# Kernel optimization log

Measured on AMD Instinct MI355X. Metric: run time of the kernel, lower is better.

## Reference

```python
import jax, jax.numpy as jnp
import numpy as np

MIN_PTS = 4

def setup_inputs() -> dict:
    key = jax.random.key(0)
    ks = jax.random.split(key, 10)
    P, N = 2048, 256            # proposals, max points per proposal slot
    H1, H2, OUT = 64, 128, 256  # PointNet MLP widths, extractor out_dim
    points = jax.random.normal(ks[0], (P, N, 3), dtype=jnp.float32)
    lengths = jax.random.randint(ks[1], (P,), 0, N, dtype=jnp.int32)  # some < MIN_PTS -> invalid
    centers = jax.random.normal(ks[2], (P, 3), dtype=jnp.float32) * 10.0
    sizes = jax.random.uniform(ks[3], (P, 3), minval=0.5, maxval=4.0, dtype=jnp.float32)
    proposals = jnp.concatenate([centers, sizes], axis=1)  # (P, 6)
    def lin(k, fan_in, fan_out):
        return jax.random.normal(k, (fan_in, fan_out), dtype=jnp.float32) * np.float32(1.0 / np.sqrt(fan_in))
    return {
        'points': points, 'lengths': lengths, 'proposals': proposals,
        'W1': lin(ks[4], 3, H1),   'b1': jnp.zeros((H1,), jnp.float32),
        'W2': lin(ks[5], H1, H2),  'b2': jnp.zeros((H2,), jnp.float32),
        'W3': lin(ks[6], H2, OUT), 'b3': jnp.zeros((OUT,), jnp.float32),
        'Wc': lin(ks[7], OUT, 1),  'bc': jnp.zeros((1,), jnp.float32),
        'Wr': lin(ks[8], OUT, 4),  'br': jnp.zeros((4,), jnp.float32),
    }

def reference(points, lengths, proposals, W1, b1, W2, b2, W3, b3, Wc, bc, Wr, br):
    P, N, _ = points.shape
    # repeat-padding: point i of proposal p maps to index i % n_p (gather form of the torch loop)
    L = jnp.maximum(lengths, 1)
    idx = jnp.arange(N, dtype=lengths.dtype)[None, :] % L[:, None]          # (P, N)
    batched = jnp.take_along_axis(points, idx[:, :, None], axis=1)         # (P, N, 3)
    # MultiPositionExtractor: box-normalized coords -> pointwise MLP -> max-pool
    centers = proposals[:, :3]
    half = proposals[:, 3:] * 0.5 + 1e-6
    local = (batched - centers[:, None, :]) / half[:, None, :]             # (P, N, 3)
    h = jax.nn.relu(local @ W1 + b1)                                       # (P, N, 64)
    h = jax.nn.relu(h @ W2 + b2)                                           # (P, N, 128)
    h = jax.nn.relu(h @ W3 + b3)                                           # (P, N, 256)
    feats = jnp.max(h, axis=1)                                             # (P, 256)
    # scatter-back: proposals with < MIN_PTS points get zero feature vector
    valid = lengths >= MIN_PTS
    feats = jnp.where(valid[:, None], feats, jnp.zeros((), feats.dtype))
    cls_logits = feats @ Wc + bc                                           # (P, 1)
    reg_deltas = feats @ Wr + br                                           # (P, 4)
    return cls_logits, reg_deltas
```

## Files before the change

kernel.cpp:

```cpp
#include <hip/hip_runtime.h>
#include <hip/hip_bf16.h>

#define MIN_PTS 4

typedef short bf16x8 __attribute__((ext_vector_type(8)));
typedef float f32x4  __attribute__((ext_vector_type(4)));

__device__ __forceinline__ ushort f2bf(float x) {
    unsigned u = __float_as_uint(x);
    u = (u + 0x7fffu + ((u >> 16) & 1u)) >> 16;
    return (ushort)u;
}

__device__ __forceinline__ uint cvt_pk_bf16(float lo, float hi) {
    union { __hip_bfloat162 h; uint u; } cv;
    cv.h = __float22bfloat162_rn(make_float2(lo, hi));
    return cv.u;
}

__global__ void pack_weights(const float* __restrict__ W2, const float* __restrict__ W3,
                             ushort* __restrict__ B2P, ushort* __restrict__ B3P)
{
    int idx = blockIdx.x * 256 + threadIdx.x;
    if (idx < 8192) {
        int j = idx & 7, l = (idx >> 3) & 63, ks = (idx >> 9) & 1, nt = idx >> 10;
        int k   = ks * 32 + (l >> 4) * 8 + j;
        int col = nt * 16 + (l & 15);
        B2P[idx] = f2bf(W2[k * 128 + col]);
    }
    if (idx < 32768) {
        int j = idx & 7, l = (idx >> 3) & 63, ks = (idx >> 9) & 3, nt = idx >> 11;
        int k   = ks * 32 + (l >> 4) * 8 + j;
        int col = nt * 16 + (l & 15);
        B3P[idx] = f2bf(W3[k * 256 + col]);
    }
}

__global__ __launch_bounds__(512, 4) void refine_loop(
    const float* __restrict__ points,
    const int*   __restrict__ lengths,
    const float* __restrict__ proposals,
    const float* __restrict__ W1, const float* __restrict__ b1,
    const float* __restrict__ b2,
    const float* __restrict__ b3,
    const ushort* __restrict__ B2P, const ushort* __restrict__ B3P,
    int* __restrict__ featsG,
    int P, int N, int work, int NB)
{
    __shared__ __align__(16) ushort A1[4096];
    __shared__ __align__(16) ushort A3[8192];

    const int tid  = threadIdx.x;
    const int lane = tid & 63;
    const int wu   = __builtin_amdgcn_readfirstlane(tid >> 6);
    const int rc   = lane & 15;
    const int g    = lane >> 4;

    float w1a[8], w1b[8], w1c[8], b1r[8];
    #pragma unroll
    for (int i = 0; i < 8; ++i) {
        const int f = wu * 8 + i;
        w1a[i] = W1[f]; w1b[i] = W1[64 + f]; w1c[i] = W1[128 + f]; b1r[i] = b1[f];
    }
    f32x4 bias2q;
    #pragma unroll
    for (int rr = 0; rr < 4; ++rr) bias2q[rr] = b2[16 * wu + 4 * g + rr];
    const float b3v0 = b3[16 * (2 * wu + 0) + rc];
    const float b3v1 = b3[16 * (2 * wu + 1) + rc];

    ushort* const a1wr = &A1[(((lane >> 4) * 2 + (wu >> 2)) * 64 + (wu & 3) * 16 + rc) * 8];
    const int ks3 = wu >> 1;
    const int g3  = (2 * wu + (g >> 1)) & 3;

    int q = blockIdx.x;
    int   lenC;
    float prC[6];
    float p0C, p1C, p2C;
    {
        const int pp = q >> 2, ss = q & 3;
        lenC = lengths[pp];
        #pragma unroll
        for (int i = 0; i < 6; ++i) prC[i] = proposals[pp * 6 + i];
        const int jj = min(ss * 64 + lane, max(lenC, 1) - 1);
        const float* pt = points + ((long)pp * N + jj) * 3;
        p0C = pt[0]; p1C = pt[1]; p2C = pt[2];
    }

    while (q < work) {
        const int   pcur   = q >> 2;
        const bool  active = (lenC >= MIN_PTS) && ((q & 3) * 64 < lenC);
        float pr[6];
        #pragma unroll
        for (int i = 0; i < 6; ++i) pr[i] = prC[i];
        const float p0 = p0C, p1 = p1C, p2 = p2C;

        const int qn = q + NB;
        if (qn < work) {
            const int pp = qn >> 2, ss = qn & 3;
            lenC = lengths[pp];
            #pragma unroll
            for (int i = 0; i < 6; ++i) prC[i] = proposals[pp * 6 + i];
            const int jj = min(ss * 64 + lane, max(lenC, 1) - 1);
            const float* pt = points + ((long)pp * N + jj) * 3;
            p0C = pt[0]; p1C = pt[1]; p2C = pt[2];
        }

        if (active) {
            {
                const float rx = __builtin_amdgcn_rcpf(fmaf(pr[3], 0.5f, 1e-6f));
                const float ry = __builtin_amdgcn_rcpf(fmaf(pr[4], 0.5f, 1e-6f));
                const float rz = __builtin_amdgcn_rcpf(fmaf(pr[5], 0.5f, 1e-6f));
                const float x0 = (p0 - pr[0]) * rx;
                const float x1 = (p1 - pr[1]) * ry;
                const float x2 = (p2 - pr[2]) * rz;
                float v[8];
                #pragma unroll
                for (int i = 0; i < 8; ++i)
                    v[i] = fmaxf(fmaf(x0, w1a[i], fmaf(x1, w1b[i], fmaf(x2, w1c[i], b1r[i]))), 0.f);
                uint4 qq;
                qq.x = cvt_pk_bf16(v[0], v[1]);
                qq.y = cvt_pk_bf16(v[2], v[3]);
                qq.z = cvt_pk_bf16(v[4], v[5]);
                qq.w = cvt_pk_bf16(v[6], v[7]);
                *(uint4*)a1wr = qq;
            }
            __syncthreads();

            {
                f32x4 acc2[4];
                #pragma unroll
                for (int mt = 0; mt < 4; ++mt) acc2[mt] = bias2q;

                #pragma unroll
                for (int ks = 0; ks < 2; ++ks) {
                    const bf16x8 bw = *(const bf16x8*)(B2P + ((wu * 2 + ks) * 64 + lane) * 8);
                    #pragma unroll
                    for (int mt = 0; mt < 4; ++mt) {
                        const bf16x8 a = *(const bf16x8*)&A1[((mt * 2 + ks) * 64 + lane) * 8];
                        acc2[mt] = __builtin_amdgcn_mfma_f32_16x16x32_bf16(bw, a, acc2[mt], 0, 0, 0);
                    }
                }
                #pragma unroll
                for (int mt = 0; mt < 4; ++mt) {
                    const uint u0 = cvt_pk_bf16(fmaxf(acc2[mt][0], 0.f), fmaxf(acc2[mt][1], 0.f));
                    const uint u1 = cvt_pk_bf16(fmaxf(acc2[mt][2], 0.f), fmaxf(acc2[mt][3], 0.f));
                    const int chunk = (mt * 4 + ks3) * 64 + g3 * 16 + rc;
                    uint2 val; val.x = u0; val.y = u1;
                    *(uint2*)&A3[chunk * 8 + (g & 1) * 4] = val;
                }
            }
            __syncthreads();

            {
                f32x4 acc3a[4], acc3b[4];
                #pragma unroll
                for (int mt = 0; mt < 4; ++mt) {
                    acc3a[mt] = (f32x4){b3v0, b3v0, b3v0, b3v0};
                    acc3b[mt] = (f32x4){b3v1, b3v1, b3v1, b3v1};
                }
                #pragma unroll
                for (int ks = 0; ks < 4; ++ks) {
                    const bf16x8 bf0 = *(const bf16x8*)(B3P + (((2 * wu + 0) * 4 + ks) * 64 + lane) * 8);
                    const bf16x8 bf1 = *(const bf16x8*)(B3P + (((2 * wu + 1) * 4 + ks) * 64 + lane) * 8);
                    #pragma unroll
                    for (int mt = 0; mt < 4; ++mt) {
                        const bf16x8 a = *(const bf16x8*)&A3[((mt * 4 + ks) * 64 + lane) * 8];
                        acc3a[mt] = __builtin_amdgcn_mfma_f32_16x16x32_bf16(a, bf0, acc3a[mt], 0, 0, 0);
                        acc3b[mt] = __builtin_amdgcn_mfma_f32_16x16x32_bf16(a, bf1, acc3b[mt], 0, 0, 0);
                    }
                }
                float pool0 = 0.f, pool1 = 0.f;
                #pragma unroll
                for (int mt = 0; mt < 4; ++mt)
                    #pragma unroll
                    for (int rr = 0; rr < 4; ++rr) {
                        pool0 = fmaxf(pool0, acc3a[mt][rr]);
                        pool1 = fmaxf(pool1, acc3b[mt][rr]);
                    }
                pool0 = fmaxf(pool0, __shfl_xor(pool0, 16, 64));
                pool0 = fmaxf(pool0, __shfl_xor(pool0, 32, 64));
                pool1 = fmaxf(pool1, __shfl_xor(pool1, 16, 64));
                pool1 = fmaxf(pool1, __shfl_xor(pool1, 32, 64));
                if (g == 0) {
                    atomicMax(&featsG[pcur * 256 + (2 * wu + 0) * 16 + rc], __float_as_int(pool0));
                    atomicMax(&featsG[pcur * 256 + (2 * wu + 1) * 16 + rc], __float_as_int(pool1));
                }
            }
        }
        q = qn;
    }
}

__global__ __launch_bounds__(256) void heads_kernel(
    const int* __restrict__ featsG,
    const float* __restrict__ Wc, const float* __restrict__ bc,
    const float* __restrict__ Wr, const float* __restrict__ br,
    float* __restrict__ out, int P)
{
    const int tid  = threadIdx.x;
    const int lane = tid & 63;
    const int p    = blockIdx.x * 4 + (tid >> 6);
    if (p >= P) return;

    const int4 vi = *(const int4*)&featsG[p * 256 + lane * 4];
    float v[4] = {__int_as_float(vi.x), __int_as_float(vi.y),
                  __int_as_float(vi.z), __int_as_float(vi.w)};

    const float4 wc = *(const float4*)&Wc[lane * 4];
    float c  = v[0] * wc.x + v[1] * wc.y + v[2] * wc.z + v[3] * wc.w;
    float r0 = 0.f, r1 = 0.f, r2 = 0.f, r3 = 0.f;
    #pragma unroll
    for (int i = 0; i < 4; ++i) {
        const float4 wr = *(const float4*)&Wr[(lane * 4 + i) * 4];
        r0 = fmaf(v[i], wr.x, r0);
        r1 = fmaf(v[i], wr.y, r1);
        r2 = fmaf(v[i], wr.z, r2);
        r3 = fmaf(v[i], wr.w, r3);
    }
    #pragma unroll
    for (int off = 32; off > 0; off >>= 1) {
        c  += __shfl_xor(c,  off, 64);
        r0 += __shfl_xor(r0, off, 64);
        r1 += __shfl_xor(r1, off, 64);
        r2 += __shfl_xor(r2, off, 64);
        r3 += __shfl_xor(r3, off, 64);
    }
    if (lane == 0) {
        out[p]             = c  + bc[0];
        out[P + p * 4 + 0] = r0 + br[0];
        out[P + p * 4 + 1] = r1 + br[1];
        out[P + p * 4 + 2] = r2 + br[2];
        out[P + p * 4 + 3] = r3 + br[3];
    }
}

extern "C" void kernel_launch(void* const* d_in, const int* in_sizes, int n_in,
                              void* d_out, int out_size, void* d_ws, size_t ws_size,
                              hipStream_t stream)
{
    const float* points    = (const float*)d_in[0];
    const int*   lengths   = (const int*)  d_in[1];
    const float* proposals = (const float*)d_in[2];
    const float* W1 = (const float*)d_in[3];
    const float* b1 = (const float*)d_in[4];
    const float* W2 = (const float*)d_in[5];
    const float* b2 = (const float*)d_in[6];
    const float* W3 = (const float*)d_in[7];
    const float* b3 = (const float*)d_in[8];
    const float* Wc = (const float*)d_in[9];
    const float* bc = (const float*)d_in[10];
    const float* Wr = (const float*)d_in[11];
    const float* br = (const float*)d_in[12];
    float* out = (float*)d_out;

    const int P = in_sizes[1];
    const int N = in_sizes[0] / (3 * P);
    const int SMAX = (N + 63) / 64;
    const int work = P * SMAX;
    const int NB   = 2048;

    ushort* B2P    = (ushort*)d_ws;
    ushort* B3P    = B2P + 8192;
    int*    featsG = (int*)((char*)d_ws + 81920);

    hipMemsetAsync(featsG, 0, (size_t)P * 256 * sizeof(int), stream);
    pack_weights<<<dim3(128), dim3(256), 0, stream>>>(W2, W3, B2P, B3P);
    refine_loop<<<dim3(NB), dim3(512), 0, stream>>>(
        points, lengths, proposals, W1, b1, b2, b3, B2P, B3P, featsG,
        P, N, work, NB);
    heads_kernel<<<dim3((P + 3) / 4), dim3(256), 0, stream>>>(
        featsG, Wc, bc, Wr, br, out, P);
}
```

Before: 61.03 us.

## Process two point slices per block with double-buffered LDS and fuse zeroing

Replaces the persistent grid-stride loop with one block per pair of 64-point slices of a proposal. Invalid or empty slices exit early, and the stages of the two slices are interleaved across double-buffered LDS, so each barrier is shared by two slices' work. The memset of the feature buffer is folded into the weight-packing kernel, which removes one launch. In exchange it launches many more blocks, doubles LDS per block (which may lower occupancy), and drops the prefetch of the next item's points.

```diff
diff --git a/kernel.cpp b/kernel.cpp
--- a/kernel.cpp
+++ b/kernel.cpp
@@ -18,8 +18,9 @@
     return cv.u;
 }
 
-__global__ void pack_weights(const float* __restrict__ W2, const float* __restrict__ W3,
-                             ushort* __restrict__ B2P, ushort* __restrict__ B3P)
+__global__ void pack_zero(const float* __restrict__ W2, const float* __restrict__ W3,
+                          ushort* __restrict__ B2P, ushort* __restrict__ B3P,
+                          int* __restrict__ featsG, int PF)
 {
     int idx = blockIdx.x * 256 + threadIdx.x;
     if (idx < 8192) {
@@ -34,9 +35,10 @@
         int col = nt * 16 + (l & 15);
         B3P[idx] = f2bf(W3[k * 256 + col]);
     }
-}
-
-__global__ __launch_bounds__(512, 4) void refine_loop(
+    if (idx < PF) featsG[idx] = 0;
+}
+
+__global__ __launch_bounds__(512, 4) void refine_pair(
     const float* __restrict__ points,
     const int*   __restrict__ lengths,
     const float* __restrict__ proposals,
@@ -45,10 +47,17 @@
     const float* __restrict__ b3,
     const ushort* __restrict__ B2P, const ushort* __restrict__ B3P,
     int* __restrict__ featsG,
-    int P, int N, int work, int NB)
-{
-    __shared__ __align__(16) ushort A1[4096];
-    __shared__ __align__(16) ushort A3[8192];
+    int P, int N)
+{
+    const int bid  = blockIdx.x;
+    const int p    = bid >> 1;
+    const int s0   = (bid & 1) * 2;
+    const int len  = lengths[p];
+    if (len < MIN_PTS || s0 * 64 >= len) return;
+    const bool act1 = (s0 + 1) * 64 < len;
+
+    __shared__ __align__(16) ushort A1[2][4096];
+    __shared__ __align__(16) ushort A3[2][8192];
 
     const int tid  = threadIdx.x;
     const int lane = tid & 63;
@@ -56,6 +65,13 @@
     const int rc   = lane & 15;
     const int g    = lane >> 4;
 
+    const float cx = proposals[p * 6 + 0];
+    const float cy = proposals[p * 6 + 1];
+    const float cz = proposals[p * 6 + 2];
+    const float rx = __builtin_amdgcn_rcpf(fmaf(proposals[p * 6 + 3], 0.5f, 1e-6f));
+    const float ry = __builtin_amdgcn_rcpf(fmaf(proposals[p * 6 + 4], 0.5f, 1e-6f));
+    const float rz = __builtin_amdgcn_rcpf(fmaf(proposals[p * 6 + 5], 0.5f, 1e-6f));
+
     float w1a[8], w1b[8], w1c[8], b1r[8];
     #pragma unroll
     for (int i = 0; i < 8; ++i) {
@@ -68,127 +84,99 @@
     const float b3v0 = b3[16 * (2 * wu + 0) + rc];
     const float b3v1 = b3[16 * (2 * wu + 1) + rc];
 
-    ushort* const a1wr = &A1[(((lane >> 4) * 2 + (wu >> 2)) * 64 + (wu & 3) * 16 + rc) * 8];
+    const int a1chunk = ((lane >> 4) * 2 + (wu >> 2)) * 64 + (wu & 3) * 16 + rc;
     const int ks3 = wu >> 1;
     const int g3  = (2 * wu + (g >> 1)) & 3;
 
-    int q = blockIdx.x;
-    int   lenC;
-    float prC[6];
-    float p0C, p1C, p2C;
-    {
-        const int pp = q >> 2, ss = q & 3;
-        lenC = lengths[pp];
-        #pragma unroll
-        for (int i = 0; i < 6; ++i) prC[i] = proposals[pp * 6 + i];
-        const int jj = min(ss * 64 + lane, max(lenC, 1) - 1);
-        const float* pt = points + ((long)pp * N + jj) * 3;
-        p0C = pt[0]; p1C = pt[1]; p2C = pt[2];
-    }
-
-    while (q < work) {
-        const int   pcur   = q >> 2;
-        const bool  active = (lenC >= MIN_PTS) && ((q & 3) * 64 < lenC);
-        float pr[6];
-        #pragma unroll
-        for (int i = 0; i < 6; ++i) pr[i] = prC[i];
-        const float p0 = p0C, p1 = p1C, p2 = p2C;
-
-        const int qn = q + NB;
-        if (qn < work) {
-            const int pp = qn >> 2, ss = qn & 3;
-            lenC = lengths[pp];
+    auto phaseA = [&](int s, int buf) {
+        const int jj = min(s * 64 + lane, len - 1);
+        const float* pt = points + ((long)p * N + jj) * 3;
+        const float x0 = (pt[0] - cx) * rx;
+        const float x1 = (pt[1] - cy) * ry;
+        const float x2 = (pt[2] - cz) * rz;
+        float v[8];
+        #pragma unroll
+        for (int i = 0; i < 8; ++i)
+            v[i] = fmaxf(fmaf(x0, w1a[i], fmaf(x1, w1b[i], fmaf(x2, w1c[i], b1r[i]))), 0.f);
+        uint4 qq;
+        qq.x = cvt_pk_bf16(v[0], v[1]);
+        qq.y = cvt_pk_bf16(v[2], v[3]);
+        qq.z = cvt_pk_bf16(v[4], v[5]);
+        qq.w = cvt_pk_bf16(v[6], v[7]);
+        *(uint4*)&A1[buf][a1chunk * 8] = qq;
+    };
+
+    auto phaseB = [&](int buf) {
+        f32x4 acc2[4];
+        #pragma unroll
+        for (int mt = 0; mt < 4; ++mt) acc2[mt] = bias2q;
+        #pragma unroll
+        for (int ks = 0; ks < 2; ++ks) {
+            const bf16x8 bw = *(const bf16x8*)(B2P + ((wu * 2 + ks) * 64 + lane) * 8);
             #pragma unroll
-            for (int i = 0; i < 6; ++i) prC[i] = proposals[pp * 6 + i];
-            const int jj = min(ss * 64 + lane, max(lenC, 1) - 1);
-            const float* pt = points + ((long)pp * N + jj) * 3;
-            p0C = pt[0]; p1C = pt[1]; p2C = pt[2];
-        }
-
-        if (active) {
-            {
-                const float rx = __builtin_amdgcn_rcpf(fmaf(pr[3], 0.5f, 1e-6f));
-                const float ry = __builtin_amdgcn_rcpf(fmaf(pr[4], 0.5f, 1e-6f));
-                const float rz = __builtin_amdgcn_rcpf(fmaf(pr[5], 0.5f, 1e-6f));
-                const float x0 = (p0 - pr[0]) * rx;
-                const float x1 = (p1 - pr[1]) * ry;
-                const float x2 = (p2 - pr[2]) * rz;
-                float v[8];
-                #pragma unroll
-                for (int i = 0; i < 8; ++i)
-                    v[i] = fmaxf(fmaf(x0, w1a[i], fmaf(x1, w1b[i], fmaf(x2, w1c[i], b1r[i]))), 0.f);
-                uint4 qq;
-                qq.x = cvt_pk_bf16(v[0], v[1]);
-                qq.y = cvt_pk_bf16(v[2], v[3]);
-                qq.z = cvt_pk_bf16(v[4], v[5]);
-                qq.w = cvt_pk_bf16(v[6], v[7]);
-                *(uint4*)a1wr = qq;
+            for (int mt = 0; mt < 4; ++mt) {
+                const bf16x8 a = *(const bf16x8*)&A1[buf][((mt * 2 + ks) * 64 + lane) * 8];
+                acc2[mt] = __builtin_amdgcn_mfma_f32_16x16x32_bf16(bw, a, acc2[mt], 0, 0, 0);
             }
-            __syncthreads();
-
-            {
-                f32x4 acc2[4];
-                #pragma unroll
-                for (int mt = 0; mt < 4; ++mt) acc2[mt] = bias2q;
-
-                #pragma unroll
-                for (int ks = 0; ks < 2; ++ks) {
-                    const bf16x8 bw = *(const bf16x8*)(B2P + ((wu * 2 + ks) * 64 + lane) * 8);
-                    #pragma unroll
-                    for (int mt = 0; mt < 4; ++mt) {
-                        const bf16x8 a = *(const bf16x8*)&A1[((mt * 2 + ks) * 64 + lane) * 8];
-                        acc2[mt] = __builtin_amdgcn_mfma_f32_16x16x32_bf16(bw, a, acc2[mt], 0, 0, 0);
-                    }
-                }
-                #pragma unroll
-                for (int mt = 0; mt < 4; ++mt) {
-                    const uint u0 = cvt_pk_bf16(fmaxf(acc2[mt][0], 0.f), fmaxf(acc2[mt][1], 0.f));
-                    const uint u1 = cvt_pk_bf16(fmaxf(acc2[mt][2], 0.f), fmaxf(acc2[mt][3], 0.f));
-                    const int chunk = (mt * 4 + ks3) * 64 + g3 * 16 + rc;
-                    uint2 val; val.x = u0; val.y = u1;
-                    *(uint2*)&A3[chunk * 8 + (g & 1) * 4] = val;
-                }
+        }
+        #pragma unroll
+        for (int mt = 0; mt < 4; ++mt) {
+            const uint u0 = cvt_pk_bf16(fmaxf(acc2[mt][0], 0.f), fmaxf(acc2[mt][1], 0.f));
+            const uint u1 = cvt_pk_bf16(fmaxf(acc2[mt][2], 0.f), fmaxf(acc2[mt][3], 0.f));
+            const int chunk = (mt * 4 + ks3) * 64 + g3 * 16 + rc;
+            uint2 val; val.x = u0; val.y = u1;
+            *(uint2*)&A3[buf][chunk * 8 + (g & 1) * 4] = val;
+        }
+    };
+
+    auto phaseD = [&](int buf) {
+        f32x4 acc3a[4], acc3b[4];
+        #pragma unroll
+        for (int mt = 0; mt < 4; ++mt) {
+            acc3a[mt] = (f32x4){b3v0, b3v0, b3v0, b3v0};
+            acc3b[mt] = (f32x4){b3v1, b3v1, b3v1, b3v1};
+        }
+        #pragma unroll
+        for (int ks = 0; ks < 4; ++ks) {
+            const bf16x8 bf0 = *(const bf16x8*)(B3P + (((2 * wu + 0) * 4 + ks) * 64 + lane) * 8);
+            const bf16x8 bf1 = *(const bf16x8*)(B3P + (((2 * wu + 1) * 4 + ks) * 64 + lane) * 8);
+            #pragma unroll
+            for (int mt = 0; mt < 4; ++mt) {
+                const bf16x8 a = *(const bf16x8*)&A3[buf][((mt * 4 + ks) * 64 + lane) * 8];
+                acc3a[mt] = __builtin_amdgcn_mfma_f32_16x16x32_bf16(a, bf0, acc3a[mt], 0, 0, 0);
+                acc3b[mt] = __builtin_amdgcn_mfma_f32_16x16x32_bf16(a, bf1, acc3b[mt], 0, 0, 0);
             }
-            __syncthreads();
-
-            {
-                f32x4 acc3a[4], acc3b[4];
-                #pragma unroll
-                for (int mt = 0; mt < 4; ++mt) {
-                    acc3a[mt] = (f32x4){b3v0, b3v0, b3v0, b3v0};
-                    acc3b[mt] = (f32x4){b3v1, b3v1, b3v1, b3v1};
-                }
-                #pragma unroll
-                for (int ks = 0; ks < 4; ++ks) {
-                    const bf16x8 bf0 = *(const bf16x8*)(B3P + (((2 * wu + 0) * 4 + ks) * 64 + lane) * 8);
-                    const bf16x8 bf1 = *(const bf16x8*)(B3P + (((2 * wu + 1) * 4 + ks) * 64 + lane) * 8);
-                    #pragma unroll
-                    for (int mt = 0; mt < 4; ++mt) {
-                        const bf16x8 a = *(const bf16x8*)&A3[((mt * 4 + ks) * 64 + lane) * 8];
-                        acc3a[mt] = __builtin_amdgcn_mfma_f32_16x16x32_bf16(a, bf0, acc3a[mt], 0, 0, 0);
-                        acc3b[mt] = __builtin_amdgcn_mfma_f32_16x16x32_bf16(a, bf1, acc3b[mt], 0, 0, 0);
-                    }
-                }
-                float pool0 = 0.f, pool1 = 0.f;
-                #pragma unroll
-                for (int mt = 0; mt < 4; ++mt)
-                    #pragma unroll
-                    for (int rr = 0; rr < 4; ++rr) {
-                        pool0 = fmaxf(pool0, acc3a[mt][rr]);
-                        pool1 = fmaxf(pool1, acc3b[mt][rr]);
-                    }
-                pool0 = fmaxf(pool0, __shfl_xor(pool0, 16, 64));
-                pool0 = fmaxf(pool0, __shfl_xor(pool0, 32, 64));
-                pool1 = fmaxf(pool1, __shfl_xor(pool1, 16, 64));
-                pool1 = fmaxf(pool1, __shfl_xor(pool1, 32, 64));
-                if (g == 0) {
-                    atomicMax(&featsG[pcur * 256 + (2 * wu + 0) * 16 + rc], __float_as_int(pool0));
-                    atomicMax(&featsG[pcur * 256 + (2 * wu + 1) * 16 + rc], __float_as_int(pool1));
-                }
+        }
+        float pool0 = 0.f, pool1 = 0.f;
+        #pragma unroll
+        for (int mt = 0; mt < 4; ++mt)
+            #pragma unroll
+            for (int rr = 0; rr < 4; ++rr) {
+                pool0 = fmaxf(pool0, acc3a[mt][rr]);
+                pool1 = fmaxf(pool1, acc3b[mt][rr]);
             }
-        }
-        q = qn;
-    }
+        pool0 = fmaxf(pool0, __shfl_xor(pool0, 16, 64));
+        pool0 = fmaxf(pool0, __shfl_xor(pool0, 32, 64));
+        pool1 = fmaxf(pool1, __shfl_xor(pool1, 16, 64));
+        pool1 = fmaxf(pool1, __shfl_xor(pool1, 32, 64));
+        if (g == 0) {
+            atomicMax(&featsG[p * 256 + (2 * wu + 0) * 16 + rc], __float_as_int(pool0));
+            atomicMax(&featsG[p * 256 + (2 * wu + 1) * 16 + rc], __float_as_int(pool1));
+        }
+    };
+
+    phaseA(s0, 0);
+    __syncthreads();
+
+    if (act1) phaseA(s0 + 1, 1);
+    phaseB(0);
+    __syncthreads();
+
+    if (act1) phaseB(1);
+    phaseD(0);
+    __syncthreads();
+
+    if (act1) phaseD(1);
 }
 
 __global__ __launch_bounds__(256) void heads_kernel(
@@ -255,19 +243,17 @@
 
     const int P = in_sizes[1];
     const int N = in_sizes[0] / (3 * P);
-    const int SMAX = (N + 63) / 64;
-    const int work = P * SMAX;
-    const int NB   = 2048;
+    const int PAIRS = ((N + 63) / 64 + 1) / 2;
 
     ushort* B2P    = (ushort*)d_ws;
     ushort* B3P    = B2P + 8192;
     int*    featsG = (int*)((char*)d_ws + 81920);
 
-    hipMemsetAsync(featsG, 0, (size_t)P * 256 * sizeof(int), stream);
-    pack_weights<<<dim3(128), dim3(256), 0, stream>>>(W2, W3, B2P, B3P);
-    refine_loop<<<dim3(NB), dim3(512), 0, stream>>>(
-        points, lengths, proposals, W1, b1, b2, b3, B2P, B3P, featsG,
-        P, N, work, NB);
+    const int PF = P * 256;
+    pack_zero<<<dim3((PF + 255) / 256), dim3(256), 0, stream>>>(
+        W2, W3, B2P, B3P, featsG, PF);
+    refine_pair<<<dim3(P * PAIRS), dim3(512), 0, stream>>>(
+        points, lengths, proposals, W1, b1, b2, b3, B2P, B3P, featsG, P, N);
     heads_kernel<<<dim3((P + 3) / 4), dim3(256), 0, stream>>>(
         featsG, Wc, bc, Wr, br, out, P);
 }
```

Result: faster. 57.30 us (-6.1%).
